# Optimization experiments

Measured on AMD Instinct MI355X. Metric: run time of the kernel, lower is better.

## Reference

```python
import jax, jax.numpy as jnp
import numpy as np

B, S, DIM = 16, 8192, 128
H, KV, D = 4, 2, 64  # heads, kv_heads, dim_head


def setup_inputs() -> dict:
    key = jax.random.key(0)
    ks = jax.random.split(key, 8)
    scale = 0.05
    return {
        "x": jax.random.normal(ks[0], (B, S, DIM), dtype=jnp.float32),
        "Wq": jax.random.normal(ks[1], (H, D, DIM), dtype=jnp.float32) * scale,
        "bq": jax.random.normal(ks[2], (H, D), dtype=jnp.float32) * scale,
        "Wk": jax.random.normal(ks[3], (KV, D, DIM), dtype=jnp.float32) * scale,
        "bk": jax.random.normal(ks[4], (KV, D), dtype=jnp.float32) * scale,
        "Wv": jax.random.normal(ks[5], (KV, D, DIM), dtype=jnp.float32) * scale,
        "bv": jax.random.normal(ks[6], (KV, D), dtype=jnp.float32) * scale,
        "Wo": jax.random.normal(ks[7], (DIM, DIM), dtype=jnp.float32) * scale,
    }


def reference(x, Wq, bq, Wk, bk, Wv, bv, Wo):
    b, s, _ = x.shape
    # MultiHeadLinear: per-head Linear stacked on last axis -> [B,S,D,H]
    q_st = jnp.einsum("bsc,hdc->bsdh", x, Wq) + bq.T  # [B,S,D,H]
    k_st = jnp.einsum("bsc,hdc->bsdh", x, Wk) + bk.T  # [B,S,D,KV]
    v_st = jnp.einsum("bsc,hdc->bsdh", x, Wv) + bv.T  # [B,S,D,KV]
    # .view(B,-1,heads,dim_head): raw reshape of (D,H) block into (H,D)
    q = q_st.reshape(b, s, H, D)
    k = k_st.reshape(b, s, KV, D)
    v = v_st.reshape(b, s, KV, D)
    # k scaled by q mean over heads (no softmax anywhere)
    k = k * jnp.mean(q, axis=2, keepdims=True)  # [B,S,KV,D]
    attn = jnp.einsum("bshd,bskd->bshk", q, k) / jnp.sqrt(jnp.asarray(D, q.dtype))
    out = jnp.einsum("bshk,bskd->bshd", attn, v)  # [B,S,H,D]
    # reshape(B,-1,dim): [B,S,H*D=256] -> [B,2S,128]
    out = out.reshape(b, -1, DIM)
    return out @ Wo.T
```

## Files before the change

### kernel.cpp

```cpp
#include <hip/hip_runtime.h>
#include <stdint.h>


using short8 = __attribute__((ext_vector_type(8))) short;
using f32x4  = __attribute__((ext_vector_type(4))) float;

constexpr int XSTR = 136;
constexpr int PSTR = 12;
constexpr int T_TILES = 8;

__device__ __forceinline__ unsigned short f2bf(float f) {
    unsigned int u = __float_as_uint(f);
    u += 0x7FFFu + ((u >> 16) & 1u);
    return (unsigned short)(u >> 16);
}

__device__ __forceinline__ void barrier_nodrain() {
    asm volatile("s_waitcnt lgkmcnt(0)\n\ts_barrier" ::: "memory");
}

__global__ void prep_weights(const float* __restrict__ Wq, const float* __restrict__ bq,
                             const float* __restrict__ Wk, const float* __restrict__ bk,
                             const float* __restrict__ Wv, const float* __restrict__ bv,
                             const float* __restrict__ Wo,
                             unsigned short* __restrict__ Wp, float* __restrict__ bias)
{
    const int ch = blockIdx.x;
    const int c  = threadIdx.x;
    float w, b;
    if (ch < 256) {
        const int hh = ch & 3, dd = ch >> 2;
        w = Wq[(hh * 64 + dd) * 128 + c];
        b = bq[hh * 64 + dd];
    } else if (ch < 384) {
        const int i = ch - 256;
        const int kvh = i & 1, dd = i >> 1;
        w = Wk[(kvh * 64 + dd) * 128 + c];
        b = bk[kvh * 64 + dd];
    } else {
        const int i  = ch - 384;
        const int jg = i >> 6, kp = (i >> 4) & 3, jm = i & 15;
        const int j  = (jg >> 1) * 32 + jm * 2 + (jg & 1);
        const int kv = kp >> 1, p = kp & 1;
        float acc = 0.f, bacc = 0.f;
        #pragma unroll 8
        for (int d = 0; d < 64; ++d) {
            const int idx = kv * 64 + d;
            const int kvh = idx & 1, dd = idx >> 1;
            const float wo = Wo[j * 128 + p * 64 + d];
            acc  += wo * Wv[(kvh * 64 + dd) * 128 + c];
            bacc += wo * bv[kvh * 64 + dd];
        }
        w = acc; b = bacc;
    }
    Wp[ch * 128 + c] = f2bf(w);
    if (c == 0) bias[ch] = b;
}

__device__ __forceinline__ void stage8_load(const float* __restrict__ x, int tb, int row0,
                                            int l, float4* xv)
{
    const int row = row0 + (l >> 3);
    const float* src = x + (size_t)(tb + row) * 128 + (l & 7) * 4;
    #pragma unroll
    for (int j = 0; j < 4; ++j) xv[j] = *(const float4*)(src + 32 * j);
}
__device__ __forceinline__ void stage8_write(unsigned short* __restrict__ xb, int row0,
                                             int l, const float4* xv)
{
    const int row = row0 + (l >> 3);
    #pragma unroll
    for (int j = 0; j < 4; ++j) {
        ushort4 s;
        s.x = f2bf(xv[j].x); s.y = f2bf(xv[j].y); s.z = f2bf(xv[j].z); s.w = f2bf(xv[j].w);
        *(ushort4*)&xb[row * XSTR + (l & 7) * 4 + 32 * j] = s;
    }
}

__global__ __launch_bounds__(512, 2)
void fused_attn_kernel(const float* __restrict__ x,
                       const unsigned short* __restrict__ Wp,
                       const float* __restrict__ bias,
                       float* __restrict__ out)
{
    __shared__ __align__(16) unsigned short xlds[3][64 * XSTR];
    __shared__ __align__(16) float partial[2][4][64][PSTR];
    __shared__ __align__(16) float coeffw[4][64][8];

    const int tid = threadIdx.x;
    const int l   = tid & 63;
    const int wv  = tid >> 6;
    const int lr  = l & 15, lg = l >> 4;
    const int tok0 = blockIdx.x * (T_TILES * 64);

    if (wv < 4) {
        const int dc = wv;
        int chb[6];
        #pragma unroll
        for (int n = 0; n < 4; ++n) chb[n] = n * 64 + dc * 16;
        chb[4] = 256 + dc * 16;
        chb[5] = 320 + dc * 16;

        short8 areg[24];
        #pragma unroll
        for (int n = 0; n < 6; ++n)
            #pragma unroll
            for (int ks = 0; ks < 4; ++ks)
                areg[n * 4 + ks] = *(const short8*)(Wp + (size_t)(chb[n] + lr) * 128 + ks * 32 + lg * 8);
        f32x4 biasv[6];
        #pragma unroll
        for (int n = 0; n < 6; ++n)
            biasv[n] = *(const f32x4*)(bias + chb[n] + lg * 4);

        auto phase1 = [&](const unsigned short* __restrict__ xb, int pb) {
            #pragma unroll
            for (int th = 0; th < 2; ++th) {
                f32x4 acc[2][6];
                #pragma unroll
                for (int ti = 0; ti < 2; ++ti)
                    #pragma unroll
                    for (int n = 0; n < 6; ++n)
                        acc[ti][n] = (f32x4){0.f, 0.f, 0.f, 0.f};
                #pragma unroll
                for (int ks = 0; ks < 4; ++ks) {
                    #pragma unroll
                    for (int ti = 0; ti < 2; ++ti) {
                        const int tf = th * 2 + ti;
                        short8 bfr = *(const short8*)&xb[(tf * 16 + lr) * XSTR + ks * 32 + lg * 8];
                        #pragma unroll
                        for (int n = 0; n < 6; ++n)
                            acc[ti][n] = __builtin_amdgcn_mfma_f32_16x16x32_bf16(
                                areg[n * 4 + ks], bfr, acc[ti][n], 0, 0, 0);
                    }
                }
                #pragma unroll
                for (int ti = 0; ti < 2; ++ti) {
                    const int tf = th * 2 + ti;
                    float pa[8];
                    #pragma unroll
                    for (int c = 0; c < 8; ++c) pa[c] = 0.f;
                    #pragma unroll
                    for (int r = 0; r < 4; ++r) {
                        const float q0 = acc[ti][0][r] + biasv[0][r];
                        const float q1 = acc[ti][1][r] + biasv[1][r];
                        const float q2 = acc[ti][2][r] + biasv[2][r];
                        const float q3 = acc[ti][3][r] + biasv[3][r];
                        const float k0v = acc[ti][4][r] + biasv[4][r];
                        const float k1v = acc[ti][5][r] + biasv[5][r];
                        const float qm  = 0.25f * (q0 + q1 + q2 + q3);
                        const float kt0 = k0v * qm, kt1 = k1v * qm;
                        pa[0] += q0 * kt0; pa[1] += q1 * kt0;
                        pa[2] += q0 * kt1; pa[3] += q1 * kt1;
                        pa[4] += q2 * kt0; pa[5] += q3 * kt0;
                        pa[6] += q2 * kt1; pa[7] += q3 * kt1;
                    }
                    #pragma unroll
                    for (int c = 0; c < 8; ++c) pa[c] += __shfl_xor(pa[c], 16);
                    #pragma unroll
                    for (int c = 0; c < 8; ++c) pa[c] += __shfl_xor(pa[c], 32);
                    if (lg == 0) {
                        f32x4 p0 = {pa[0], pa[1], pa[2], pa[3]};
                        f32x4 p1 = {pa[4], pa[5], pa[6], pa[7]};
                        float* dst = &partial[pb][dc][tf * 16 + lr][0];
                        *(f32x4*)(dst)     = p0;
                        *(f32x4*)(dst + 4) = p1;
                    }
                }
            }
        };

        {
            float4 xv[4];
            stage8_load(x, tok0, wv * 8, l, xv);
            stage8_write(xlds[0], wv * 8, l, xv);
        }
        barrier_nodrain();
        phase1(xlds[0], 0);
        barrier_nodrain();

        for (int t = 0; t < T_TILES; ++t) {
            float4 xv[4];
            const bool do_stage = (t < T_TILES - 2);
            if (do_stage) stage8_load(x, tok0 + (t + 2) * 64, wv * 8, l, xv);
            if (t < T_TILES - 1) phase1(xlds[(t + 1) % 3], (t + 1) & 1);
            if (do_stage) stage8_write(xlds[(t + 2) % 3], wv * 8, l, xv);
            barrier_nodrain();
        }
    } else {
        const int jgp = wv - 4;

        short8 breg[32];
        #pragma unroll
        for (int j2 = 0; j2 < 2; ++j2)
            #pragma unroll
            for (int kp = 0; kp < 4; ++kp)
                #pragma unroll
                for (int ks = 0; ks < 4; ++ks)
                    breg[(j2 * 4 + kp) * 4 + ks] = *(const short8*)
                        (Wp + (size_t)(384 + (jgp * 2 + j2) * 64 + kp * 16 + lr) * 128 + ks * 32 + lg * 8);
        float bvv[2][4];
        #pragma unroll
        for (int j2 = 0; j2 < 2; ++j2)
            #pragma unroll
            for (int kp = 0; kp < 4; ++kp)
                bvv[j2][kp] = bias[384 + (jgp * 2 + j2) * 64 + kp * 16 + lr];

        auto phase2 = [&](const unsigned short* __restrict__ xb, int t) {
            const int g0    = tok0 + t * 64;
            const int bb    = g0 >> 13;
            const int srow0 = bb * 16384 + 2 * (g0 & 8191);
            #pragma unroll
            for (int mf = 0; mf < 4; ++mf) {
                f32x4 a2[2][4];
                #pragma unroll
                for (int j2 = 0; j2 < 2; ++j2)
                    #pragma unroll
                    for (int kp = 0; kp < 4; ++kp)
                        a2[j2][kp] = (f32x4){0.f, 0.f, 0.f, 0.f};
                #pragma unroll
                for (int ks = 0; ks < 4; ++ks) {
                    short8 af = *(const short8*)&xb[(mf * 16 + lr) * XSTR + ks * 32 + lg * 8];
                    #pragma unroll
                    for (int j2 = 0; j2 < 2; ++j2)
                        #pragma unroll
                        for (int kp = 0; kp < 4; ++kp)
                            a2[j2][kp] = __builtin_amdgcn_mfma_f32_16x16x32_bf16(
                                af, breg[(j2 * 4 + kp) * 4 + ks], a2[j2][kp], 0, 0, 0);
                }
                #pragma unroll
                for (int r = 0; r < 4; ++r) {
                    const int tokL = lg * 4 + r;
                    const int tok  = mf * 16 + tokL;
                    f32x4 cl = *(const f32x4*)&coeffw[jgp][tok][0];
                    f32x4 ch = *(const f32x4*)&coeffw[jgp][tok][4];
                    float2 s0, s1;
                    {
                        const float a0 = a2[0][0][r] + bvv[0][0];
                        const float a1 = a2[0][1][r] + bvv[0][1];
                        const float av = a2[0][2][r] + bvv[0][2];
                        const float a3 = a2[0][3][r] + bvv[0][3];
                        s0.x = cl[0] * a0 + cl[1] * a1 + cl[2] * av + cl[3] * a3;
                        s1.x = ch[0] * a0 + ch[1] * a1 + ch[2] * av + ch[3] * a3;
                    }
                    {
                        const float a0 = a2[1][0][r] + bvv[1][0];
                        const float a1 = a2[1][1][r] + bvv[1][1];
                        const float av = a2[1][2][r] + bvv[1][2];
                        const float a3 = a2[1][3][r] + bvv[1][3];
                        s0.y = cl[0] * a0 + cl[1] * a1 + cl[2] * av + cl[3] * a3;
                        s1.y = ch[0] * a0 + ch[1] * a1 + ch[2] * av + ch[3] * a3;
                    }
                    const int row = srow0 + 32 * mf + 2 * tokL;
                    float* dst = out + (size_t)row * 128 + jgp * 32 + lr * 2;
                    *(float2*)(dst)       = s0;
                    *(float2*)(dst + 128) = s1;
                }
            }
        };

        {
            float4 xv[4];
            stage8_load(x, tok0, 32 + jgp * 8, l, xv);
            stage8_write(xlds[0], 32 + jgp * 8, l, xv);
        }
        barrier_nodrain();
        {
            float4 xv[4];
            stage8_load(x, tok0 + 64, jgp * 16, l, xv);
            stage8_write(xlds[1], jgp * 16, l, xv);
            stage8_load(x, tok0 + 64, jgp * 16 + 8, l, xv);
            stage8_write(xlds[1], jgp * 16 + 8, l, xv);
        }
        barrier_nodrain();

        for (int t = 0; t < T_TILES; ++t) {
            float4 xv[4];
            const bool do_stage = (t < T_TILES - 2);
            if (do_stage) stage8_load(x, tok0 + (t + 2) * 64, 32 + jgp * 8, l, xv);
            {
                const int pb = t & 1;
                float s[8];
                #pragma unroll
                for (int c = 0; c < 8; ++c) s[c] = 0.f;
                #pragma unroll
                for (int dcc = 0; dcc < 4; ++dcc) {
                    const float* pr = &partial[pb][dcc][l][0];
                    #pragma unroll
                    for (int c = 0; c < 8; ++c) s[c] += pr[c];
                }
                f32x4 c0 = {s[0] * 0.125f, s[1] * 0.125f, s[2] * 0.125f, s[3] * 0.125f};
                f32x4 c1 = {s[4] * 0.125f, s[5] * 0.125f, s[6] * 0.125f, s[7] * 0.125f};
                *(f32x4*)&coeffw[jgp][l][0] = c0;
                *(f32x4*)&coeffw[jgp][l][4] = c1;
            }
            phase2(xlds[t % 3], t);
            if (do_stage) stage8_write(xlds[(t + 2) % 3], 32 + jgp * 8, l, xv);
            barrier_nodrain();
        }
    }
}

extern "C" void kernel_launch(void* const* d_in, const int* in_sizes, int n_in,
                              void* d_out, int out_size, void* d_ws, size_t ws_size,
                              hipStream_t stream)
{
    (void)in_sizes; (void)n_in; (void)out_size; (void)ws_size;
    const float* x  = (const float*)d_in[0];
    const float* Wq = (const float*)d_in[1];
    const float* bq = (const float*)d_in[2];
    const float* Wk = (const float*)d_in[3];
    const float* bk = (const float*)d_in[4];
    const float* Wv = (const float*)d_in[5];
    const float* bv = (const float*)d_in[6];
    const float* Wo = (const float*)d_in[7];

    unsigned short* Wp   = (unsigned short*)d_ws;
    float*          bias = (float*)((char*)d_ws + 896 * 128 * 2);

    prep_weights<<<896, 128, 0, stream>>>(Wq, bq, Wk, bk, Wv, bv, Wo, Wp, bias);
    fused_attn_kernel<<<256, 512, 0, stream>>>(x, Wp, bias, (float*)d_out);
}
```

Baseline: 56.35 us.

## Split output projection across eight consumer waves with 768-thread blocks

The block grows from 512 to 768 threads (4 producer waves computing q/k coefficients, 8 consumer waves computing the fused V·Wo output). Each consumer wave now handles 16 output columns instead of 32, which halves its B-fragment register footprint and MFMA work per tile. All x staging moves to the consumer waves. Coefficients now go into a single shared array, and outputs are written with nontemporal scalar stores. The aim is more parallel MFMA issue and lower register pressure per wave. In exchange, occupancy drops to one block per CU and the stores become narrower.

```diff
diff --git a/kernel.cpp b/kernel.cpp
--- a/kernel.cpp
+++ b/kernel.cpp
@@ -6,7 +6,7 @@
 using f32x4  = __attribute__((ext_vector_type(4))) float;
 
 constexpr int XSTR = 136;
-constexpr int PSTR = 12;
+constexpr int PSTR = 10;
 constexpr int T_TILES = 8;
 
 __device__ __forceinline__ unsigned short f2bf(float f) {
@@ -40,7 +40,7 @@
     } else {
         const int i  = ch - 384;
         const int jg = i >> 6, kp = (i >> 4) & 3, jm = i & 15;
-        const int j  = (jg >> 1) * 32 + jm * 2 + (jg & 1);
+        const int j  = jg * 16 + jm;
         const int kv = kp >> 1, p = kp & 1;
         float acc = 0.f, bacc = 0.f;
         #pragma unroll 8
@@ -77,7 +77,7 @@
     }
 }
 
-__global__ __launch_bounds__(512, 2)
+__global__ __launch_bounds__(768, 1)
 void fused_attn_kernel(const float* __restrict__ x,
                        const unsigned short* __restrict__ Wp,
                        const float* __restrict__ bias,
@@ -85,7 +85,7 @@
 {
     __shared__ __align__(16) unsigned short xlds[3][64 * XSTR];
     __shared__ __align__(16) float partial[2][4][64][PSTR];
-    __shared__ __align__(16) float coeffw[4][64][8];
+    __shared__ __align__(16) float coeff[64][8];
 
     const int tid = threadIdx.x;
     const int l   = tid & 63;
@@ -114,169 +114,91 @@
 
         auto phase1 = [&](const unsigned short* __restrict__ xb, int pb) {
             #pragma unroll
-            for (int th = 0; th < 2; ++th) {
-                f32x4 acc[2][6];
-                #pragma unroll
-                for (int ti = 0; ti < 2; ++ti)
+            for (int p = 0; p < 4; ++p) {
+                f32x4 acc[6];
+                #pragma unroll
+                for (int n = 0; n < 6; ++n) acc[n] = (f32x4){0.f, 0.f, 0.f, 0.f};
+                #pragma unroll
+                for (int ks = 0; ks < 4; ++ks) {
+                    short8 bfr = *(const short8*)&xb[(p * 16 + lr) * XSTR + ks * 32 + lg * 8];
                     #pragma unroll
                     for (int n = 0; n < 6; ++n)
-                        acc[ti][n] = (f32x4){0.f, 0.f, 0.f, 0.f};
-                #pragma unroll
-                for (int ks = 0; ks < 4; ++ks) {
-                    #pragma unroll
-                    for (int ti = 0; ti < 2; ++ti) {
-                        const int tf = th * 2 + ti;
-                        short8 bfr = *(const short8*)&xb[(tf * 16 + lr) * XSTR + ks * 32 + lg * 8];
-                        #pragma unroll
-                        for (int n = 0; n < 6; ++n)
-                            acc[ti][n] = __builtin_amdgcn_mfma_f32_16x16x32_bf16(
-                                areg[n * 4 + ks], bfr, acc[ti][n], 0, 0, 0);
-                    }
-                }
-                #pragma unroll
-                for (int ti = 0; ti < 2; ++ti) {
-                    const int tf = th * 2 + ti;
-                    float pa[8];
-                    #pragma unroll
-                    for (int c = 0; c < 8; ++c) pa[c] = 0.f;
-                    #pragma unroll
-                    for (int r = 0; r < 4; ++r) {
-                        const float q0 = acc[ti][0][r] + biasv[0][r];
-                        const float q1 = acc[ti][1][r] + biasv[1][r];
-                        const float q2 = acc[ti][2][r] + biasv[2][r];
-                        const float q3 = acc[ti][3][r] + biasv[3][r];
-                        const float k0v = acc[ti][4][r] + biasv[4][r];
-                        const float k1v = acc[ti][5][r] + biasv[5][r];
-                        const float qm  = 0.25f * (q0 + q1 + q2 + q3);
-                        const float kt0 = k0v * qm, kt1 = k1v * qm;
-                        pa[0] += q0 * kt0; pa[1] += q1 * kt0;
-                        pa[2] += q0 * kt1; pa[3] += q1 * kt1;
-                        pa[4] += q2 * kt0; pa[5] += q3 * kt0;
-                        pa[6] += q2 * kt1; pa[7] += q3 * kt1;
-                    }
-                    #pragma unroll
-                    for (int c = 0; c < 8; ++c) pa[c] += __shfl_xor(pa[c], 16);
-                    #pragma unroll
-                    for (int c = 0; c < 8; ++c) pa[c] += __shfl_xor(pa[c], 32);
-                    if (lg == 0) {
-                        f32x4 p0 = {pa[0], pa[1], pa[2], pa[3]};
-                        f32x4 p1 = {pa[4], pa[5], pa[6], pa[7]};
-                        float* dst = &partial[pb][dc][tf * 16 + lr][0];
-                        *(f32x4*)(dst)     = p0;
-                        *(f32x4*)(dst + 4) = p1;
-                    }
+                        acc[n] = __builtin_amdgcn_mfma_f32_16x16x32_bf16(
+                            areg[n * 4 + ks], bfr, acc[n], 0, 0, 0);
+                }
+                float pa[8];
+                #pragma unroll
+                for (int c = 0; c < 8; ++c) pa[c] = 0.f;
+                #pragma unroll
+                for (int r = 0; r < 4; ++r) {
+                    const float q0 = acc[0][r] + biasv[0][r];
+                    const float q1 = acc[1][r] + biasv[1][r];
+                    const float q2 = acc[2][r] + biasv[2][r];
+                    const float q3 = acc[3][r] + biasv[3][r];
+                    const float k0v = acc[4][r] + biasv[4][r];
+                    const float k1v = acc[5][r] + biasv[5][r];
+                    const float qm  = 0.25f * (q0 + q1 + q2 + q3);
+                    const float kt0 = k0v * qm, kt1 = k1v * qm;
+                    pa[0] += q0 * kt0; pa[1] += q1 * kt0;
+                    pa[2] += q0 * kt1; pa[3] += q1 * kt1;
+                    pa[4] += q2 * kt0; pa[5] += q3 * kt0;
+                    pa[6] += q2 * kt1; pa[7] += q3 * kt1;
+                }
+                #pragma unroll
+                for (int c = 0; c < 8; ++c) pa[c] += __shfl_xor(pa[c], 16);
+                #pragma unroll
+                for (int c = 0; c < 8; ++c) pa[c] += __shfl_xor(pa[c], 32);
+                if (lg == 0) {
+                    float* dst = &partial[pb][dc][p * 16 + lr][0];
+                    *(float2*)(dst)     = make_float2(pa[0], pa[1]);
+                    *(float2*)(dst + 2) = make_float2(pa[2], pa[3]);
+                    *(float2*)(dst + 4) = make_float2(pa[4], pa[5]);
+                    *(float2*)(dst + 6) = make_float2(pa[6], pa[7]);
                 }
             }
         };
 
+        barrier_nodrain();
+        phase1(xlds[0], 0);
+        barrier_nodrain();
+
+        for (int t = 0; t < T_TILES; ++t) {
+            if (t < T_TILES - 1) phase1(xlds[(t + 1) % 3], (t + 1) & 1);
+            barrier_nodrain();
+        }
+    } else {
+        const int jg = wv - 4;
+
+        short8 breg[16];
+        #pragma unroll
+        for (int kp = 0; kp < 4; ++kp)
+            #pragma unroll
+            for (int ks = 0; ks < 4; ++ks)
+                breg[kp * 4 + ks] = *(const short8*)
+                    (Wp + (size_t)(384 + jg * 64 + kp * 16 + lr) * 128 + ks * 32 + lg * 8);
+        float bvv[4];
+        #pragma unroll
+        for (int kp = 0; kp < 4; ++kp)
+            bvv[kp] = bias[384 + jg * 64 + kp * 16 + lr];
+
         {
             float4 xv[4];
-            stage8_load(x, tok0, wv * 8, l, xv);
-            stage8_write(xlds[0], wv * 8, l, xv);
-        }
-        barrier_nodrain();
-        phase1(xlds[0], 0);
+            stage8_load(x, tok0, jg * 8, l, xv);
+            stage8_write(xlds[0], jg * 8, l, xv);
+        }
+        barrier_nodrain();
+        {
+            float4 xv[4];
+            stage8_load(x, tok0 + 64, jg * 8, l, xv);
+            stage8_write(xlds[1], jg * 8, l, xv);
+        }
         barrier_nodrain();
 
         for (int t = 0; t < T_TILES; ++t) {
             float4 xv[4];
             const bool do_stage = (t < T_TILES - 2);
-            if (do_stage) stage8_load(x, tok0 + (t + 2) * 64, wv * 8, l, xv);
-            if (t < T_TILES - 1) phase1(xlds[(t + 1) % 3], (t + 1) & 1);
-            if (do_stage) stage8_write(xlds[(t + 2) % 3], wv * 8, l, xv);
-            barrier_nodrain();
-        }
-    } else {
-        const int jgp = wv - 4;
-
-        short8 breg[32];
-        #pragma unroll
-        for (int j2 = 0; j2 < 2; ++j2)
-            #pragma unroll
-            for (int kp = 0; kp < 4; ++kp)
-                #pragma unroll
-                for (int ks = 0; ks < 4; ++ks)
-                    breg[(j2 * 4 + kp) * 4 + ks] = *(const short8*)
-                        (Wp + (size_t)(384 + (jgp * 2 + j2) * 64 + kp * 16 + lr) * 128 + ks * 32 + lg * 8);
-        float bvv[2][4];
-        #pragma unroll
-        for (int j2 = 0; j2 < 2; ++j2)
-            #pragma unroll
-            for (int kp = 0; kp < 4; ++kp)
-                bvv[j2][kp] = bias[384 + (jgp * 2 + j2) * 64 + kp * 16 + lr];
-
-        auto phase2 = [&](const unsigned short* __restrict__ xb, int t) {
-            const int g0    = tok0 + t * 64;
-            const int bb    = g0 >> 13;
-            const int srow0 = bb * 16384 + 2 * (g0 & 8191);
-            #pragma unroll
-            for (int mf = 0; mf < 4; ++mf) {
-                f32x4 a2[2][4];
-                #pragma unroll
-                for (int j2 = 0; j2 < 2; ++j2)
-                    #pragma unroll
-                    for (int kp = 0; kp < 4; ++kp)
-                        a2[j2][kp] = (f32x4){0.f, 0.f, 0.f, 0.f};
-                #pragma unroll
-                for (int ks = 0; ks < 4; ++ks) {
-                    short8 af = *(const short8*)&xb[(mf * 16 + lr) * XSTR + ks * 32 + lg * 8];
-                    #pragma unroll
-                    for (int j2 = 0; j2 < 2; ++j2)
-                        #pragma unroll
-                        for (int kp = 0; kp < 4; ++kp)
-                            a2[j2][kp] = __builtin_amdgcn_mfma_f32_16x16x32_bf16(
-                                af, breg[(j2 * 4 + kp) * 4 + ks], a2[j2][kp], 0, 0, 0);
-                }
-                #pragma unroll
-                for (int r = 0; r < 4; ++r) {
-                    const int tokL = lg * 4 + r;
-                    const int tok  = mf * 16 + tokL;
-                    f32x4 cl = *(const f32x4*)&coeffw[jgp][tok][0];
-                    f32x4 ch = *(const f32x4*)&coeffw[jgp][tok][4];
-                    float2 s0, s1;
-                    {
-                        const float a0 = a2[0][0][r] + bvv[0][0];
-                        const float a1 = a2[0][1][r] + bvv[0][1];
-                        const float av = a2[0][2][r] + bvv[0][2];
-                        const float a3 = a2[0][3][r] + bvv[0][3];
-                        s0.x = cl[0] * a0 + cl[1] * a1 + cl[2] * av + cl[3] * a3;
-                        s1.x = ch[0] * a0 + ch[1] * a1 + ch[2] * av + ch[3] * a3;
-                    }
-                    {
-                        const float a0 = a2[1][0][r] + bvv[1][0];
-                        const float a1 = a2[1][1][r] + bvv[1][1];
-                        const float av = a2[1][2][r] + bvv[1][2];
-                        const float a3 = a2[1][3][r] + bvv[1][3];
-                        s0.y = cl[0] * a0 + cl[1] * a1 + cl[2] * av + cl[3] * a3;
-                        s1.y = ch[0] * a0 + ch[1] * a1 + ch[2] * av + ch[3] * a3;
-                    }
-                    const int row = srow0 + 32 * mf + 2 * tokL;
-                    float* dst = out + (size_t)row * 128 + jgp * 32 + lr * 2;
-                    *(float2*)(dst)       = s0;
-                    *(float2*)(dst + 128) = s1;
-                }
-            }
-        };
-
-        {
-            float4 xv[4];
-            stage8_load(x, tok0, 32 + jgp * 8, l, xv);
-            stage8_write(xlds[0], 32 + jgp * 8, l, xv);
-        }
-        barrier_nodrain();
-        {
-            float4 xv[4];
-            stage8_load(x, tok0 + 64, jgp * 16, l, xv);
-            stage8_write(xlds[1], jgp * 16, l, xv);
-            stage8_load(x, tok0 + 64, jgp * 16 + 8, l, xv);
-            stage8_write(xlds[1], jgp * 16 + 8, l, xv);
-        }
-        barrier_nodrain();
-
-        for (int t = 0; t < T_TILES; ++t) {
-            float4 xv[4];
-            const bool do_stage = (t < T_TILES - 2);
-            if (do_stage) stage8_load(x, tok0 + (t + 2) * 64, 32 + jgp * 8, l, xv);
+            if (do_stage) stage8_load(x, tok0 + (t + 2) * 64, jg * 8, l, xv);
+
             {
                 const int pb = t & 1;
                 float s[8];
@@ -286,15 +208,56 @@
                 for (int dcc = 0; dcc < 4; ++dcc) {
                     const float* pr = &partial[pb][dcc][l][0];
                     #pragma unroll
-                    for (int c = 0; c < 8; ++c) s[c] += pr[c];
-                }
-                f32x4 c0 = {s[0] * 0.125f, s[1] * 0.125f, s[2] * 0.125f, s[3] * 0.125f};
-                f32x4 c1 = {s[4] * 0.125f, s[5] * 0.125f, s[6] * 0.125f, s[7] * 0.125f};
-                *(f32x4*)&coeffw[jgp][l][0] = c0;
-                *(f32x4*)&coeffw[jgp][l][4] = c1;
+                    for (int c = 0; c < 4; ++c) {
+                        float2 v = *(const float2*)(pr + 2 * c);
+                        s[2 * c] += v.x; s[2 * c + 1] += v.y;
+                    }
+                }
+                float* cw = &coeff[l][0];
+                *(float2*)(cw)     = make_float2(s[0] * 0.125f, s[1] * 0.125f);
+                *(float2*)(cw + 2) = make_float2(s[2] * 0.125f, s[3] * 0.125f);
+                *(float2*)(cw + 4) = make_float2(s[4] * 0.125f, s[5] * 0.125f);
+                *(float2*)(cw + 6) = make_float2(s[6] * 0.125f, s[7] * 0.125f);
             }
-            phase2(xlds[t % 3], t);
-            if (do_stage) stage8_write(xlds[(t + 2) % 3], 32 + jgp * 8, l, xv);
+
+            {
+                const unsigned short* xb = xlds[t % 3];
+                const int g0    = tok0 + t * 64;
+                const int bb    = g0 >> 13;
+                const int srow0 = bb * 16384 + 2 * (g0 & 8191);
+                #pragma unroll
+                for (int mf = 0; mf < 4; ++mf) {
+                    f32x4 acc[4];
+                    #pragma unroll
+                    for (int kp = 0; kp < 4; ++kp) acc[kp] = (f32x4){0.f, 0.f, 0.f, 0.f};
+                    #pragma unroll
+                    for (int ks = 0; ks < 4; ++ks) {
+                        short8 af = *(const short8*)&xb[(mf * 16 + lr) * XSTR + ks * 32 + lg * 8];
+                        #pragma unroll
+                        for (int kp = 0; kp < 4; ++kp)
+                            acc[kp] = __builtin_amdgcn_mfma_f32_16x16x32_bf16(
+                                af, breg[kp * 4 + ks], acc[kp], 0, 0, 0);
+                    }
+                    #pragma unroll
+                    for (int r = 0; r < 4; ++r) {
+                        const int tok = mf * 16 + lg * 4 + r;
+                        f32x4 cl = *(const f32x4*)&coeff[tok][0];
+                        f32x4 ch = *(const f32x4*)&coeff[tok][4];
+                        const float a0 = acc[0][r] + bvv[0];
+                        const float a1 = acc[1][r] + bvv[1];
+                        const float a2 = acc[2][r] + bvv[2];
+                        const float a3 = acc[3][r] + bvv[3];
+                        const float o0 = cl[0] * a0 + cl[1] * a1 + cl[2] * a2 + cl[3] * a3;
+                        const float o1 = ch[0] * a0 + ch[1] * a1 + ch[2] * a2 + ch[3] * a3;
+                        const int row = srow0 + 32 * mf + 2 * (lg * 4 + r);
+                        float* dst = out + (size_t)row * 128 + jg * 16 + lr;
+                        __builtin_nontemporal_store(o0, dst);
+                        __builtin_nontemporal_store(o1, dst + 128);
+                    }
+                }
+            }
+
+            if (do_stage) stage8_write(xlds[(t + 2) % 3], jg * 8, l, xv);
             barrier_nodrain();
         }
     }
@@ -318,5 +281,5 @@
     float*          bias = (float*)((char*)d_ws + 896 * 128 * 2);
 
     prep_weights<<<896, 128, 0, stream>>>(Wq, bq, Wk, bk, Wv, bv, Wo, Wp, bias);
-    fused_attn_kernel<<<256, 512, 0, stream>>>(x, Wp, bias, (float*)d_out);
-}
+    fused_attn_kernel<<<256, 768, 0, stream>>>(x, Wp, bias, (float*)d_out);
+}
```

Result: slower. 58.88 us (+4.5%).
